# Kernel optimization log

Hardware: AMD Instinct MI355X
Metric: run time of the kernel (lower is better)

Reference implementation:

```python
import jax, jax.numpy as jnp
import numpy as np

B = 1024        # batch
S = 2048        # nsampled + 1 (index 0 is the positive label)
E = 128         # emb_size
V = 100000      # vocab = len(tags_weight)


def setup_inputs() -> dict:
    key = jax.random.key(0)
    k1, k2, k3, k4 = jax.random.split(key, 4)
    inputs = jax.random.normal(k1, (B, E), dtype=jnp.float32)
    weight = jax.random.normal(k2, (V, E), dtype=jnp.float32)
    bias = jax.random.normal(k3, (V,), dtype=jnp.float32)
    sample_ids = jax.random.randint(k4, (B, S), 0, V)  # column 0 = positive label
    return {"inputs": inputs, "weight": weight, "bias": bias, "sample_ids": sample_ids}


def reference(inputs, weight, bias, sample_ids):
    # Gather sampled rows: [B, S, E] and [B, S]
    sample_weights = weight[sample_ids]
    sample_bias = bias[sample_ids]
    # Batched dot: logits[b, s] = <inputs[b], sample_weights[b, s]> + bias
    logits = jnp.einsum('be,bse->bs', inputs, sample_weights) + sample_bias
    # CrossEntropyLoss with targets all-zero (positive class is at index 0), mean reduction
    loss = jnp.mean(jax.nn.logsumexp(logits, axis=-1) - logits[:, 0])
    return loss
```

## Files before the change

### kernel.cpp

```cpp
#include <hip/hip_runtime.h>
#include <float.h>
#include <math.h>

#define BATCH 1024
#define NS    2048
#define EMB   128
#define VOCAB 100000
#define THREADS 256
#define CHUNKS 4
#define SCHUNK (NS / CHUNKS)
#define ITERS  (SCHUNK / 32)

#define FCHUNKS 8
#define FSCHUNK (NS / FCHUNKS)
#define ITERSF (FSCHUNK / 64)

#define KSHIFT 40.0f
#define INVB   (1.0f / (float)BATCH)


typedef float floatx2 __attribute__((ext_vector_type(2)));

#if __has_builtin(__builtin_amdgcn_cvt_pk_f32_fp8) && __has_builtin(__builtin_amdgcn_cvt_pk_fp8_f32)
#define USE_FP8_BUILTINS 1
#else
#define USE_FP8_BUILTINS 0
#include <hip/hip_fp8.h>
#endif

__device__ inline floatx2 cvt2_lo(unsigned int w) {
#if USE_FP8_BUILTINS
    return __builtin_amdgcn_cvt_pk_f32_fp8((int)w, false);
#else
    __hip_fp8_e4m3 a, b;
    a.__x = (unsigned char)(w & 0xff);
    b.__x = (unsigned char)((w >> 8) & 0xff);
    floatx2 r; r.x = (float)a; r.y = (float)b; return r;
#endif
}
__device__ inline floatx2 cvt2_hi(unsigned int w) {
#if USE_FP8_BUILTINS
    return __builtin_amdgcn_cvt_pk_f32_fp8((int)w, true);
#else
    __hip_fp8_e4m3 a, b;
    a.__x = (unsigned char)((w >> 16) & 0xff);
    b.__x = (unsigned char)((w >> 24) & 0xff);
    floatx2 r; r.x = (float)a; r.y = (float)b; return r;
#endif
}
__device__ inline unsigned int pack4_fp8(float4 v) {
#if USE_FP8_BUILTINS
    int w = 0;
    w = __builtin_amdgcn_cvt_pk_fp8_f32(v.x, v.y, w, false);
    w = __builtin_amdgcn_cvt_pk_fp8_f32(v.z, v.w, w, true);
    return (unsigned int)w;
#else
    __hip_fp8_e4m3 h0(v.x), h1(v.y), h2(v.z), h3(v.w);
    return (unsigned int)h0.__x | ((unsigned int)h1.__x << 8)
         | ((unsigned int)h2.__x << 16) | ((unsigned int)h3.__x << 24);
#endif
}

__global__ __launch_bounds__(THREADS) void convert_weights_fp8(
    const float* __restrict__ w, unsigned int* __restrict__ w8)
{
    const size_t i = (size_t)blockIdx.x * THREADS + threadIdx.x;
    const float4* src = (const float4*)w;
    float4 a = src[4 * i + 0];
    float4 b = src[4 * i + 1];
    float4 c = src[4 * i + 2];
    float4 d = src[4 * i + 3];
    uint4 o;
    o.x = pack4_fp8(a);
    o.y = pack4_fp8(b);
    o.z = pack4_fp8(c);
    o.w = pack4_fp8(d);
    ((uint4*)w8)[i] = o;
}

__global__ __launch_bounds__(THREADS, 2) void sampled_ce_partial_8(
    const float*        __restrict__ inputs,
    const unsigned int* __restrict__ w8,
    const float*        __restrict__ bias,
    const int*          __restrict__ sample_ids,
    float* __restrict__ pm,
    float* __restrict__ plogit0)
{
    const int blk   = blockIdx.x;
    const int b     = blk >> 2;
    const int chunk = blk & (CHUNKS - 1);
    const int t = threadIdx.x;
    const int e_part = t & 7;
    const int s_sub  = t >> 3;

    __shared__ float s_in[EMB];
    __shared__ int   s_ids[SCHUNK];
    __shared__ float s_red[4];

    const int* ids_row = sample_ids + (size_t)b * NS + chunk * SCHUNK;

    if (t < EMB / 4) {
        ((float4*)s_in)[t] = ((const float4*)(inputs + (size_t)b * EMB))[t];
    }
    if (t >= 64 && t < 64 + SCHUNK / 4) {
        ((int4*)s_ids)[t - 64] = ((const int4*)ids_row)[t - 64];
    }
    __syncthreads();

    int ids[ITERS];
#pragma unroll
    for (int it = 0; it < ITERS; ++it) ids[it] = s_ids[it * 32 + s_sub];

    uint4 q[ITERS];
#pragma unroll
    for (int it = 0; it < ITERS; ++it) {
        q[it] = ((const uint4*)w8)[(size_t)ids[it] * 8 + e_part];
    }
    float bv[ITERS];
#pragma unroll
    for (int it = 0; it < ITERS; ++it) bv[it] = bias[ids[it]];

    floatx2 cin[8];
#pragma unroll
    for (int p = 0; p < 8; ++p) {
        const int base = e_part * 16 + 2 * p;
        cin[p].x = s_in[base];
        cin[p].y = s_in[base + 1];
    }

    float lsum = 0.0f;
    float l0 = 0.0f;
#pragma unroll
    for (int it = 0; it < ITERS; ++it) {
        floatx2 a2 = {0.0f, 0.0f};
        a2 += cvt2_lo(q[it].x) * cin[0];
        a2 += cvt2_hi(q[it].x) * cin[1];
        a2 += cvt2_lo(q[it].y) * cin[2];
        a2 += cvt2_hi(q[it].y) * cin[3];
        a2 += cvt2_lo(q[it].z) * cin[4];
        a2 += cvt2_hi(q[it].z) * cin[5];
        a2 += cvt2_lo(q[it].w) * cin[6];
        a2 += cvt2_hi(q[it].w) * cin[7];
        float a = a2.x + a2.y;
        a += __shfl_xor(a, 1, 64);
        a += __shfl_xor(a, 2, 64);
        a += __shfl_xor(a, 4, 64);
        const float logit = a + bv[it];
        if (it == 0) l0 = logit;
        lsum += __expf(logit - KSHIFT);
    }

    if (chunk == 0 && t == 0) plogit0[b] = l0;

#pragma unroll
    for (int off = 1; off < 64; off <<= 1) lsum += __shfl_xor(lsum, off, 64);

    const int wave = t >> 6;
    if ((t & 63) == 0) s_red[wave] = lsum;
    __syncthreads();

    if (t == 0) {
        pm[blk] = (s_red[0] + s_red[1] + s_red[2] + s_red[3]) * 0.125f;
    }
}

__global__ __launch_bounds__(1024) void sampled_ce_finalize_8(
    const float* __restrict__ pm,
    const float* __restrict__ plogit0,
    float* __restrict__ out)
{
    const int t = threadIdx.x;

    const float4 p = ((const float4*)pm)[t];
    const float S = p.x + p.y + p.z + p.w;
    float v = (KSHIFT + __logf(S) - plogit0[t]) * INVB;

#pragma unroll
    for (int off = 1; off < 64; off <<= 1) v += __shfl_xor(v, off, 64);

    __shared__ float s[16];
    if ((t & 63) == 0) s[t >> 6] = v;
    __syncthreads();

    if (t == 0) {
        float sum = 0.0f;
#pragma unroll
        for (int w = 0; w < 16; ++w) sum += s[w];
        out[0] = sum;
    }
}

__global__ __launch_bounds__(THREADS) void sampled_ce_partial_f(
    const float* __restrict__ inputs,
    const float* __restrict__ weight,
    const float* __restrict__ bias,
    const int*   __restrict__ sample_ids,
    float* __restrict__ pm,
    float* __restrict__ pl,
    float* __restrict__ plogit0)
{
    const int blk   = blockIdx.x;
    const int b     = blk >> 3;
    const int chunk = blk & (FCHUNKS - 1);
    const int t = threadIdx.x;
    const int e_part  = t & 3;
    const int s_local = t >> 2;

    __shared__ float s_in[EMB];
    __shared__ float s_red[8];

    if (t < EMB / 4) {
        ((float4*)s_in)[t] = ((const float4*)(inputs + (size_t)b * EMB))[t];
    }
    const int* ids_row = sample_ids + (size_t)b * NS + chunk * FSCHUNK;
    int ids[ITERSF];
#pragma unroll
    for (int it = 0; it < ITERSF; ++it) ids[it] = ids_row[it * 64 + s_local];

    __syncthreads();

    float4 cin[8];
#pragma unroll
    for (int k = 0; k < 8; ++k) cin[k] = ((const float4*)s_in)[k * 4 + e_part];

    float m = -FLT_MAX;
    float l = 0.0f;

#pragma unroll
    for (int it = 0; it < ITERSF; ++it) {
        const int id = ids[it];
        const float4* wr = (const float4*)(weight + (size_t)id * EMB);
        float acc = 0.0f;
#pragma unroll
        for (int k = 0; k < 8; ++k) {
            float4 w = wr[k * 4 + e_part];
            acc += w.x * cin[k].x + w.y * cin[k].y + w.z * cin[k].z + w.w * cin[k].w;
        }
        acc += __shfl_xor(acc, 1, 64);
        acc += __shfl_xor(acc, 2, 64);
        const float logit = acc + bias[id];
        const float nm = fmaxf(m, logit);
        l = l * __expf(m - nm) + __expf(logit - nm);
        m = nm;
        if (chunk == 0 && it == 0 && t == 0) plogit0[b] = logit;
    }

    if (e_part != 0) { m = -FLT_MAX; l = 0.0f; }
#pragma unroll
    for (int off = 1; off < 64; off <<= 1) {
        const float om = __shfl_xor(m, off, 64);
        const float ol = __shfl_xor(l, off, 64);
        const float nm = fmaxf(m, om);
        l = l * __expf(m - nm) + ol * __expf(om - nm);
        m = nm;
    }
    const int wave = t >> 6;
    if ((t & 63) == 0) { s_red[wave * 2] = m; s_red[wave * 2 + 1] = l; }
    __syncthreads();
    if (t == 0) {
        float M = s_red[0], L = s_red[1];
#pragma unroll
        for (int w = 1; w < 4; ++w) {
            const float om = s_red[w * 2], ol = s_red[w * 2 + 1];
            const float nm = fmaxf(M, om);
            L = L * __expf(M - nm) + ol * __expf(om - nm);
            M = nm;
        }
        pm[blk] = M;
        pl[blk] = L;
    }
}

__global__ __launch_bounds__(1024) void sampled_ce_finalize_f(
    const float* __restrict__ pm,
    const float* __restrict__ pl,
    const float* __restrict__ plogit0,
    float* __restrict__ out)
{
    const int t = threadIdx.x;

    float M = pm[t * FCHUNKS + 0];
    float L = pl[t * FCHUNKS + 0];
#pragma unroll
    for (int c = 1; c < FCHUNKS; ++c) {
        const float om = pm[t * FCHUNKS + c];
        const float ol = pl[t * FCHUNKS + c];
        const float nm = fmaxf(M, om);
        L = L * __expf(M - nm) + ol * __expf(om - nm);
        M = nm;
    }
    float v = (M + __logf(L) - plogit0[t]) * INVB;

#pragma unroll
    for (int off = 1; off < 64; off <<= 1) v += __shfl_xor(v, off, 64);

    __shared__ float s[16];
    if ((t & 63) == 0) s[t >> 6] = v;
    __syncthreads();

    if (t == 0) {
        float sum = 0.0f;
#pragma unroll
        for (int w = 0; w < 16; ++w) sum += s[w];
        out[0] = sum;
    }
}

extern "C" void kernel_launch(void* const* d_in, const int* in_sizes, int n_in,
                              void* d_out, int out_size, void* d_ws, size_t ws_size,
                              hipStream_t stream) {
    const float* inputs     = (const float*)d_in[0];
    const float* weight     = (const float*)d_in[1];
    const float* bias       = (const float*)d_in[2];
    const int*   sample_ids = (const int*)d_in[3];
    float* out = (float*)d_out;

    float* ws = (float*)d_ws;
    float* pm      = ws;
    float* plogit0 = ws + BATCH * CHUNKS;
    float* fb_pm   = ws;
    float* fb_pl   = ws + BATCH * FCHUNKS;
    float* fb_pl0  = ws + 2 * BATCH * FCHUNKS;
    const size_t red_bytes = (size_t)(2 * BATCH * FCHUNKS + BATCH) * sizeof(float);
    const size_t w8_bytes  = (size_t)VOCAB * EMB;
    unsigned int* w8 = (unsigned int*)((char*)d_ws + red_bytes);

    if (ws_size >= red_bytes + w8_bytes) {
        convert_weights_fp8<<<dim3((VOCAB * EMB) / (16 * THREADS)), dim3(THREADS), 0, stream>>>(
            weight, w8);
        sampled_ce_partial_8<<<dim3(BATCH * CHUNKS), dim3(THREADS), 0, stream>>>(
            inputs, w8, bias, sample_ids, pm, plogit0);
        sampled_ce_finalize_8<<<dim3(1), dim3(1024), 0, stream>>>(pm, plogit0, out);
    } else {
        sampled_ce_partial_f<<<dim3(BATCH * FCHUNKS), dim3(THREADS), 0, stream>>>(
            inputs, weight, bias, sample_ids, fb_pm, fb_pl, fb_pl0);
        sampled_ce_finalize_f<<<dim3(1), dim3(1024), 0, stream>>>(fb_pm, fb_pl, fb_pl0, out);
    }
}
```

Before: 131.6 us.

## Fuse fp8 conversion, partial logsumexp and finalize into one cooperative kernel

Replaces the three-kernel sequence (weight fp8 conversion, per-chunk partial sums, finalize) with a single cooperative kernel of 512 blocks that uses grid syncs between the phases. Each block now handles a whole batch row, processing samples in phases of 16 gathered loads per thread, and writes per-row loss terms that block 0 reduces at the end. This removes two kernel launch gaps and the partial-sum round trip, but drops to fewer blocks with less parallelism per row, adds two grid-wide barriers, and depends on the cooperative launch succeeding; otherwise it falls back to the old path.

Measured after the change: 428.1 us. +225.3%, slower.

```diff
diff --git a/kernel.cpp b/kernel.cpp
--- a/kernel.cpp
+++ b/kernel.cpp
@@ -1,16 +1,23 @@
 #include <hip/hip_runtime.h>
+#include <hip/hip_cooperative_groups.h>
 #include <float.h>
 #include <math.h>
+
+namespace cg = cooperative_groups;
 
 #define BATCH 1024
 #define NS    2048
 #define EMB   128
 #define VOCAB 100000
 #define THREADS 256
+
+#define COOP_GRID 512
+#define CDEPTH 16
+#define CPHASES (NS / 32 / CDEPTH)
+
 #define CHUNKS 4
 #define SCHUNK (NS / CHUNKS)
 #define ITERS  (SCHUNK / 32)
-
 #define FCHUNKS 8
 #define FSCHUNK (NS / FCHUNKS)
 #define ITERSF (FSCHUNK / 64)
@@ -59,6 +66,129 @@
     return (unsigned int)h0.__x | ((unsigned int)h1.__x << 8)
          | ((unsigned int)h2.__x << 16) | ((unsigned int)h3.__x << 24);
 #endif
+}
+
+__global__ __launch_bounds__(THREADS, 2) void sampled_ce_fused(
+    const float*  __restrict__ inputs,
+    const float*  __restrict__ weight,
+    const float*  __restrict__ bias,
+    const int*    __restrict__ sample_ids,
+    unsigned int* __restrict__ w8,
+    float*        __restrict__ vrow,
+    float*        __restrict__ out)
+{
+    cg::grid_group gg = cg::this_grid();
+    const int t = threadIdx.x;
+
+    {
+        const int total = VOCAB * EMB / 16;
+        const float4* src = (const float4*)weight;
+        for (int i = blockIdx.x * THREADS + t; i < total; i += COOP_GRID * THREADS) {
+            float4 a = src[4 * i + 0];
+            float4 b = src[4 * i + 1];
+            float4 c = src[4 * i + 2];
+            float4 d = src[4 * i + 3];
+            uint4 o;
+            o.x = pack4_fp8(a);
+            o.y = pack4_fp8(b);
+            o.z = pack4_fp8(c);
+            o.w = pack4_fp8(d);
+            ((uint4*)w8)[i] = o;
+        }
+    }
+    __threadfence();
+    gg.sync();
+    __threadfence();
+
+    const int e_part = t & 7;
+    const int s_sub  = t >> 3;
+
+    __shared__ float s_in[EMB];
+    __shared__ int   s_ids[NS];
+    __shared__ float s_red[4];
+
+    for (int b = blockIdx.x; b < BATCH; b += COOP_GRID) {
+        __syncthreads();
+
+        if (t < EMB / 4) {
+            ((float4*)s_in)[t] = ((const float4*)(inputs + (size_t)b * EMB))[t];
+        }
+        const int4* ids4 = (const int4*)(sample_ids + (size_t)b * NS);
+        ((int4*)s_ids)[t]       = ids4[t];
+        ((int4*)s_ids)[t + 256] = ids4[t + 256];
+        __syncthreads();
+
+        floatx2 cin[8];
+#pragma unroll
+        for (int p = 0; p < 8; ++p) {
+            const int base = e_part * 16 + 2 * p;
+            cin[p].x = s_in[base];
+            cin[p].y = s_in[base + 1];
+        }
+
+        float lsum = 0.0f;
+        float l0 = 0.0f;
+#pragma unroll
+        for (int ph = 0; ph < CPHASES; ++ph) {
+            int ids[CDEPTH];
+#pragma unroll
+            for (int it = 0; it < CDEPTH; ++it)
+                ids[it] = s_ids[(ph * CDEPTH + it) * 32 + s_sub];
+
+            uint4 q[CDEPTH];
+#pragma unroll
+            for (int it = 0; it < CDEPTH; ++it)
+                q[it] = ((const uint4*)w8)[(size_t)ids[it] * 8 + e_part];
+            float bv[CDEPTH];
+#pragma unroll
+            for (int it = 0; it < CDEPTH; ++it) bv[it] = bias[ids[it]];
+
+#pragma unroll
+            for (int it = 0; it < CDEPTH; ++it) {
+                floatx2 a2 = {0.0f, 0.0f};
+                a2 += cvt2_lo(q[it].x) * cin[0];
+                a2 += cvt2_hi(q[it].x) * cin[1];
+                a2 += cvt2_lo(q[it].y) * cin[2];
+                a2 += cvt2_hi(q[it].y) * cin[3];
+                a2 += cvt2_lo(q[it].z) * cin[4];
+                a2 += cvt2_hi(q[it].z) * cin[5];
+                a2 += cvt2_lo(q[it].w) * cin[6];
+                a2 += cvt2_hi(q[it].w) * cin[7];
+                float a = a2.x + a2.y;
+                a += __shfl_xor(a, 1, 64);
+                a += __shfl_xor(a, 2, 64);
+                a += __shfl_xor(a, 4, 64);
+                const float logit = a + bv[it];
+                if (ph == 0 && it == 0) l0 = logit;
+                lsum += __expf(logit - KSHIFT);
+            }
+        }
+
+#pragma unroll
+        for (int off = 1; off < 64; off <<= 1) lsum += __shfl_xor(lsum, off, 64);
+        const int wave = t >> 6;
+        if ((t & 63) == 0) s_red[wave] = lsum;
+        __syncthreads();
+
+        if (t == 0) {
+            const float S = (s_red[0] + s_red[1] + s_red[2] + s_red[3]) * 0.125f;
+            vrow[b] = KSHIFT + __logf(S) - l0;
+        }
+    }
+    __threadfence();
+    gg.sync();
+    __threadfence();
+
+    if (blockIdx.x == 0) {
+        const float4 p = ((const float4*)vrow)[t];
+        float v = (p.x + p.y + p.z + p.w) * INVB;
+#pragma unroll
+        for (int off = 1; off < 64; off <<= 1) v += __shfl_xor(v, off, 64);
+        __shared__ float s2[4];
+        if ((t & 63) == 0) s2[t >> 6] = v;
+        __syncthreads();
+        if (t == 0) out[0] = s2[0] + s2[1] + s2[2] + s2[3];
+    }
 }
 
 __global__ __launch_bounds__(THREADS) void convert_weights_fp8(
@@ -98,7 +228,6 @@
     __shared__ float s_red[4];
 
     const int* ids_row = sample_ids + (size_t)b * NS + chunk * SCHUNK;
-
     if (t < EMB / 4) {
         ((float4*)s_in)[t] = ((const float4*)(inputs + (size_t)b * EMB))[t];
     }
@@ -110,12 +239,10 @@
     int ids[ITERS];
 #pragma unroll
     for (int it = 0; it < ITERS; ++it) ids[it] = s_ids[it * 32 + s_sub];
-
     uint4 q[ITERS];
 #pragma unroll
-    for (int it = 0; it < ITERS; ++it) {
+    for (int it = 0; it < ITERS; ++it)
         q[it] = ((const uint4*)w8)[(size_t)ids[it] * 8 + e_part];
-    }
     float bv[ITERS];
 #pragma unroll
     for (int it = 0; it < ITERS; ++it) bv[it] = bias[ids[it]];
@@ -128,8 +255,7 @@
         cin[p].y = s_in[base + 1];
     }
 
-    float lsum = 0.0f;
-    float l0 = 0.0f;
+    float lsum = 0.0f, l0 = 0.0f;
 #pragma unroll
     for (int it = 0; it < ITERS; ++it) {
         floatx2 a2 = {0.0f, 0.0f};
@@ -149,19 +275,14 @@
         if (it == 0) l0 = logit;
         lsum += __expf(logit - KSHIFT);
     }
-
     if (chunk == 0 && t == 0) plogit0[b] = l0;
 
 #pragma unroll
     for (int off = 1; off < 64; off <<= 1) lsum += __shfl_xor(lsum, off, 64);
-
     const int wave = t >> 6;
     if ((t & 63) == 0) s_red[wave] = lsum;
     __syncthreads();
-
-    if (t == 0) {
-        pm[blk] = (s_red[0] + s_red[1] + s_red[2] + s_red[3]) * 0.125f;
-    }
+    if (t == 0) pm[blk] = (s_red[0] + s_red[1] + s_red[2] + s_red[3]) * 0.125f;
 }
 
 __global__ __launch_bounds__(1024) void sampled_ce_finalize_8(
@@ -170,18 +291,14 @@
     float* __restrict__ out)
 {
     const int t = threadIdx.x;
-
     const float4 p = ((const float4*)pm)[t];
     const float S = p.x + p.y + p.z + p.w;
     float v = (KSHIFT + __logf(S) - plogit0[t]) * INVB;
-
 #pragma unroll
     for (int off = 1; off < 64; off <<= 1) v += __shfl_xor(v, off, 64);
-
     __shared__ float s[16];
     if ((t & 63) == 0) s[t >> 6] = v;
     __syncthreads();
-
     if (t == 0) {
         float sum = 0.0f;
 #pragma unroll
@@ -216,16 +333,13 @@
     int ids[ITERSF];
 #pragma unroll
     for (int it = 0; it < ITERSF; ++it) ids[it] = ids_row[it * 64 + s_local];
-
     __syncthreads();
 
     float4 cin[8];
 #pragma unroll
     for (int k = 0; k < 8; ++k) cin[k] = ((const float4*)s_in)[k * 4 + e_part];
 
-    float m = -FLT_MAX;
-    float l = 0.0f;
-
+    float m = -FLT_MAX, l = 0.0f;
 #pragma unroll
     for (int it = 0; it < ITERSF; ++it) {
         const int id = ids[it];
@@ -244,7 +358,6 @@
         m = nm;
         if (chunk == 0 && it == 0 && t == 0) plogit0[b] = logit;
     }
-
     if (e_part != 0) { m = -FLT_MAX; l = 0.0f; }
 #pragma unroll
     for (int off = 1; off < 64; off <<= 1) {
@@ -278,7 +391,6 @@
     float* __restrict__ out)
 {
     const int t = threadIdx.x;
-
     float M = pm[t * FCHUNKS + 0];
     float L = pl[t * FCHUNKS + 0];
 #pragma unroll
@@ -290,14 +402,11 @@
         M = nm;
     }
     float v = (M + __logf(L) - plogit0[t]) * INVB;
-
 #pragma unroll
     for (int off = 1; off < 64; off <<= 1) v += __shfl_xor(v, off, 64);
-
     __shared__ float s[16];
     if ((t & 63) == 0) s[t >> 6] = v;
     __syncthreads();
-
     if (t == 0) {
         float sum = 0.0f;
 #pragma unroll
@@ -316,6 +425,7 @@
     float* out = (float*)d_out;
 
     float* ws = (float*)d_ws;
+    float* vrow    = ws;
     float* pm      = ws;
     float* plogit0 = ws + BATCH * CHUNKS;
     float* fb_pm   = ws;
@@ -326,11 +436,20 @@
     unsigned int* w8 = (unsigned int*)((char*)d_ws + red_bytes);
 
     if (ws_size >= red_bytes + w8_bytes) {
-        convert_weights_fp8<<<dim3((VOCAB * EMB) / (16 * THREADS)), dim3(THREADS), 0, stream>>>(
-            weight, w8);
-        sampled_ce_partial_8<<<dim3(BATCH * CHUNKS), dim3(THREADS), 0, stream>>>(
-            inputs, w8, bias, sample_ids, pm, plogit0);
-        sampled_ce_finalize_8<<<dim3(1), dim3(1024), 0, stream>>>(pm, plogit0, out);
+        void* kargs[] = {
+            (void*)&inputs, (void*)&weight, (void*)&bias, (void*)&sample_ids,
+            (void*)&w8, (void*)&vrow, (void*)&out
+        };
+        hipError_t err = hipLaunchCooperativeKernel(
+            (const void*)sampled_ce_fused, dim3(COOP_GRID), dim3(THREADS),
+            kargs, 0, stream);
+        if (err != hipSuccess) {
+            convert_weights_fp8<<<dim3((VOCAB * EMB) / (16 * THREADS)), dim3(THREADS), 0, stream>>>(
+                weight, w8);
+            sampled_ce_partial_8<<<dim3(BATCH * CHUNKS), dim3(THREADS), 0, stream>>>(
+                inputs, w8, bias, sample_ids, pm, plogit0);
+            sampled_ce_finalize_8<<<dim3(1), dim3(1024), 0, stream>>>(pm, plogit0, out);
+        }
     } else {
         sampled_ce_partial_f<<<dim3(BATCH * FCHUNKS), dim3(THREADS), 0, stream>>>(
             inputs, weight, bias, sample_ids, fb_pm, fb_pl, fb_pl0);
```

## Partition sampled ids by vocab range so each block gathers a cache-local slice

Applied to the files above, without the earlier changes.

Each block now loads all 2048 sample ids for its batch row and compacts into shared memory only those falling in one of eight vocab ranges, using ballot/popcount and a shared atomic counter. It then gathers and scores only those rows, so concurrently running blocks touch a smaller region of the fp8 weight table and should hit cache more often. The cost is that every block scans the full id row, uses more shared memory, and runs a data-dependent loop with per-slot bounds checks. The finalize kernel now sums eight partials per row instead of four.

After: 146.6 us. +11.4%, slower.

```diff
diff --git a/kernel.cpp b/kernel.cpp
--- a/kernel.cpp
+++ b/kernel.cpp
@@ -7,9 +7,9 @@
 #define EMB   128
 #define VOCAB 100000
 #define THREADS 256
-#define CHUNKS 4
-#define SCHUNK (NS / CHUNKS)
-#define ITERS  (SCHUNK / 32)
+
+#define PARTS 8
+#define PSIZE (VOCAB / PARTS)
 
 #define FCHUNKS 8
 #define FSCHUNK (NS / FCHUNKS)
@@ -78,7 +78,7 @@
     ((uint4*)w8)[i] = o;
 }
 
-__global__ __launch_bounds__(THREADS, 2) void sampled_ce_partial_8(
+__global__ __launch_bounds__(THREADS, 2) void sampled_ce_partial_p(
     const float*        __restrict__ inputs,
     const unsigned int* __restrict__ w8,
     const float*        __restrict__ bias,
@@ -86,79 +86,105 @@
     float* __restrict__ pm,
     float* __restrict__ plogit0)
 {
-    const int blk   = blockIdx.x;
-    const int b     = blk >> 2;
-    const int chunk = blk & (CHUNKS - 1);
-    const int t = threadIdx.x;
+    const int blk = blockIdx.x;
+    const int p   = blk & (PARTS - 1);
+    const int b   = blk >> 3;
+    const int t   = threadIdx.x;
+    const int lane = t & 63;
     const int e_part = t & 7;
     const int s_sub  = t >> 3;
+    const int lo  = p * PSIZE;
 
     __shared__ float s_in[EMB];
-    __shared__ int   s_ids[SCHUNK];
+    __shared__ int   s_ids[NS];
+    __shared__ int   s_sel[NS];
     __shared__ float s_red[4];
-
-    const int* ids_row = sample_ids + (size_t)b * NS + chunk * SCHUNK;
+    __shared__ int   s_cnt;
+    __shared__ int   s_pos0;
 
     if (t < EMB / 4) {
         ((float4*)s_in)[t] = ((const float4*)(inputs + (size_t)b * EMB))[t];
     }
-    if (t >= 64 && t < 64 + SCHUNK / 4) {
-        ((int4*)s_ids)[t - 64] = ((const int4*)ids_row)[t - 64];
-    }
-    __syncthreads();
-
-    int ids[ITERS];
-#pragma unroll
-    for (int it = 0; it < ITERS; ++it) ids[it] = s_ids[it * 32 + s_sub];
-
-    uint4 q[ITERS];
-#pragma unroll
-    for (int it = 0; it < ITERS; ++it) {
-        q[it] = ((const uint4*)w8)[(size_t)ids[it] * 8 + e_part];
-    }
-    float bv[ITERS];
-#pragma unroll
-    for (int it = 0; it < ITERS; ++it) bv[it] = bias[ids[it]];
+    const int4* ids4 = (const int4*)(sample_ids + (size_t)b * NS);
+    ((int4*)s_ids)[t]       = ids4[t];
+    ((int4*)s_ids)[t + 256] = ids4[t + 256];
+    if (t == 0) { s_cnt = 0; s_pos0 = -1; }
+    __syncthreads();
+
+#pragma unroll
+    for (int c = 0; c < NS / THREADS; ++c) {
+        const int pos = c * THREADS + t;
+        const int id  = s_ids[pos];
+        const bool pred = ((unsigned)(id - lo)) < (unsigned)PSIZE;
+        const unsigned long long mask = __ballot(pred);
+        int base;
+        if (lane == 0) base = atomicAdd(&s_cnt, (int)__popcll(mask));
+        base = __shfl(base, 0, 64);
+        if (pred) {
+            const int slot = base +
+                (int)__popcll(mask & ((1ull << lane) - 1ull));
+            s_sel[slot] = id;
+            if (pos == 0) s_pos0 = slot;
+        }
+    }
+    __syncthreads();
+
+    const int count = s_cnt;
+    const int pos0  = s_pos0;
 
     floatx2 cin[8];
 #pragma unroll
-    for (int p = 0; p < 8; ++p) {
-        const int base = e_part * 16 + 2 * p;
-        cin[p].x = s_in[base];
-        cin[p].y = s_in[base + 1];
+    for (int q = 0; q < 8; ++q) {
+        const int base = e_part * 16 + 2 * q;
+        cin[q].x = s_in[base];
+        cin[q].y = s_in[base + 1];
     }
 
     float lsum = 0.0f;
-    float l0 = 0.0f;
-#pragma unroll
-    for (int it = 0; it < ITERS; ++it) {
-        floatx2 a2 = {0.0f, 0.0f};
-        a2 += cvt2_lo(q[it].x) * cin[0];
-        a2 += cvt2_hi(q[it].x) * cin[1];
-        a2 += cvt2_lo(q[it].y) * cin[2];
-        a2 += cvt2_hi(q[it].y) * cin[3];
-        a2 += cvt2_lo(q[it].z) * cin[4];
-        a2 += cvt2_hi(q[it].z) * cin[5];
-        a2 += cvt2_lo(q[it].w) * cin[6];
-        a2 += cvt2_hi(q[it].w) * cin[7];
-        float a = a2.x + a2.y;
-        a += __shfl_xor(a, 1, 64);
-        a += __shfl_xor(a, 2, 64);
-        a += __shfl_xor(a, 4, 64);
-        const float logit = a + bv[it];
-        if (it == 0) l0 = logit;
-        lsum += __expf(logit - KSHIFT);
-    }
-
-    if (chunk == 0 && t == 0) plogit0[b] = l0;
+    for (int base = 0; base < count; base += 8 * 32) {
+        int ids8[8];
+#pragma unroll
+        for (int it = 0; it < 8; ++it) {
+            const int slot = base + it * 32 + s_sub;
+            ids8[it] = (slot < count) ? s_sel[slot] : lo;
+        }
+        uint4 q[8];
+#pragma unroll
+        for (int it = 0; it < 8; ++it)
+            q[it] = ((const uint4*)w8)[(size_t)ids8[it] * 8 + e_part];
+        float bv[8];
+#pragma unroll
+        for (int it = 0; it < 8; ++it) bv[it] = bias[ids8[it]];
+
+#pragma unroll
+        for (int it = 0; it < 8; ++it) {
+            floatx2 a2 = {0.0f, 0.0f};
+            a2 += cvt2_lo(q[it].x) * cin[0];
+            a2 += cvt2_hi(q[it].x) * cin[1];
+            a2 += cvt2_lo(q[it].y) * cin[2];
+            a2 += cvt2_hi(q[it].y) * cin[3];
+            a2 += cvt2_lo(q[it].z) * cin[4];
+            a2 += cvt2_hi(q[it].z) * cin[5];
+            a2 += cvt2_lo(q[it].w) * cin[6];
+            a2 += cvt2_hi(q[it].w) * cin[7];
+            float a = a2.x + a2.y;
+            a += __shfl_xor(a, 1, 64);
+            a += __shfl_xor(a, 2, 64);
+            a += __shfl_xor(a, 4, 64);
+            const float logit = a + bv[it];
+            const int slot = base + it * 32 + s_sub;
+            if (slot < count) {
+                lsum += __expf(logit - KSHIFT);
+                if (slot == pos0 && e_part == 0) plogit0[b] = logit;
+            }
+        }
+    }
 
 #pragma unroll
     for (int off = 1; off < 64; off <<= 1) lsum += __shfl_xor(lsum, off, 64);
-
     const int wave = t >> 6;
     if ((t & 63) == 0) s_red[wave] = lsum;
     __syncthreads();
-
     if (t == 0) {
         pm[blk] = (s_red[0] + s_red[1] + s_red[2] + s_red[3]) * 0.125f;
     }
@@ -171,8 +197,10 @@
 {
     const int t = threadIdx.x;
 
-    const float4 p = ((const float4*)pm)[t];
-    const float S = p.x + p.y + p.z + p.w;
+    const float4* p4 = (const float4*)(pm + (size_t)t * PARTS);
+    const float4 p0 = p4[0];
+    const float4 p1 = p4[1];
+    const float S = (p0.x + p0.y + p0.z + p0.w) + (p1.x + p1.y + p1.z + p1.w);
     float v = (KSHIFT + __logf(S) - plogit0[t]) * INVB;
 
 #pragma unroll
@@ -216,16 +244,13 @@
     int ids[ITERSF];
 #pragma unroll
     for (int it = 0; it < ITERSF; ++it) ids[it] = ids_row[it * 64 + s_local];
-
     __syncthreads();
 
     float4 cin[8];
 #pragma unroll
     for (int k = 0; k < 8; ++k) cin[k] = ((const float4*)s_in)[k * 4 + e_part];
 
-    float m = -FLT_MAX;
-    float l = 0.0f;
-
+    float m = -FLT_MAX, l = 0.0f;
 #pragma unroll
     for (int it = 0; it < ITERSF; ++it) {
         const int id = ids[it];
@@ -244,7 +269,6 @@
         m = nm;
         if (chunk == 0 && it == 0 && t == 0) plogit0[b] = logit;
     }
-
     if (e_part != 0) { m = -FLT_MAX; l = 0.0f; }
 #pragma unroll
     for (int off = 1; off < 64; off <<= 1) {
@@ -278,7 +302,6 @@
     float* __restrict__ out)
 {
     const int t = threadIdx.x;
-
     float M = pm[t * FCHUNKS + 0];
     float L = pl[t * FCHUNKS + 0];
 #pragma unroll
@@ -290,14 +313,11 @@
         M = nm;
     }
     float v = (M + __logf(L) - plogit0[t]) * INVB;
-
 #pragma unroll
     for (int off = 1; off < 64; off <<= 1) v += __shfl_xor(v, off, 64);
-
     __shared__ float s[16];
     if ((t & 63) == 0) s[t >> 6] = v;
     __syncthreads();
-
     if (t == 0) {
         float sum = 0.0f;
 #pragma unroll
@@ -317,7 +337,7 @@
 
     float* ws = (float*)d_ws;
     float* pm      = ws;
-    float* plogit0 = ws + BATCH * CHUNKS;
+    float* plogit0 = ws + BATCH * PARTS;
     float* fb_pm   = ws;
     float* fb_pl   = ws + BATCH * FCHUNKS;
     float* fb_pl0  = ws + 2 * BATCH * FCHUNKS;
@@ -328,7 +348,7 @@
     if (ws_size >= red_bytes + w8_bytes) {
         convert_weights_fp8<<<dim3((VOCAB * EMB) / (16 * THREADS)), dim3(THREADS), 0, stream>>>(
             weight, w8);
-        sampled_ce_partial_8<<<dim3(BATCH * CHUNKS), dim3(THREADS), 0, stream>>>(
+        sampled_ce_partial_p<<<dim3(BATCH * PARTS), dim3(THREADS), 0, stream>>>(
             inputs, w8, bias, sample_ids, pm, plogit0);
         sampled_ce_finalize_8<<<dim3(1), dim3(1024), 0, stream>>>(pm, plogit0, out);
     } else {
```
